# Performance work log

Measured on AMD Instinct MI355X. Metric: run time of the kernel, lower is better.

## Reference

```python
import jax, jax.numpy as jnp
import numpy as np
import math

DIM_PER_HEAD = 64

def setup_inputs() -> dict:
    key = jax.random.key(0)
    k1, k2, k3, k4 = jax.random.split(key, 4)
    B, H, S, D = 2, 16, 2048, 64
    mat1 = jax.random.normal(k1, (B, H, S, D), dtype=jnp.float32)
    mat2 = jax.random.normal(k2, (B, H, S, D), dtype=jnp.float32)
    mat3 = jax.random.normal(k3, (B, H, S, D), dtype=jnp.float32)
    bias = jax.random.normal(k4, (1, 1, S, S), dtype=jnp.float32)
    return {"mat1": mat1, "mat2": mat2, "mat3": mat3, "bias": bias}

def reference(mat1, mat2, mat3, bias) -> jnp.ndarray:
    # scale Q, scores = QK^T + bias, softmax over last dim, then @ V
    scale = 1.0 / math.sqrt(DIM_PER_HEAD)
    qk = jnp.einsum('bhqd,bhkd->bhqk', mat1 * scale, mat2)  # [B,H,S,S]
    scores = jax.nn.softmax(qk + bias, axis=-1)
    return jnp.einsum('bhqk,bhkd->bhqd', scores, mat3)
```

## Files before the change

### kernel.cpp

```cpp
#include <hip/hip_runtime.h>
#include <hip/hip_bf16.h>


#define SEQ 2048
#define DH  64
#define BHN 32
#define PST 72
#define LOG2E 1.44269504088896f

typedef __attribute__((ext_vector_type(8))) short bf16x8;
typedef __attribute__((ext_vector_type(4))) float f32x4;
typedef __attribute__((ext_vector_type(8))) short short8v;

__device__ inline short f2b(float x) {
    union { float f; unsigned u; } v; v.f = x;
    unsigned r = v.u + 0x7fff + ((v.u >> 16) & 1);
    return (short)(r >> 16);
}

__device__ inline void gl_lds16(const void* g, void* l) {
    __builtin_amdgcn_global_load_lds(
        (const __attribute__((address_space(1))) void*)g,
        (__attribute__((address_space(3))) void*)l, 16, 0, 0);
}

__global__ __launch_bounds__(256)
void prep_k(const float* __restrict__ K, short* __restrict__ Kb) {
    size_t i = ((size_t)blockIdx.x * 256 + threadIdx.x) * 8;
    f32x4 a = *(const f32x4*)(K + i);
    f32x4 b = *(const f32x4*)(K + i + 4);
    short8v t;
    #pragma unroll
    for (int j = 0; j < 4; ++j) { t[j] = f2b(a[j]); t[4 + j] = f2b(b[j]); }
    *(short8v*)(Kb + i) = t;
}

__global__ __launch_bounds__(256)
void prep_v(const float* __restrict__ V, short* __restrict__ Vt) {
    __shared__ short t[64 * 72];
    const int tid = threadIdx.x;
    const int bh = blockIdx.x >> 5, st = blockIdx.x & 31, s0 = st * 64;
    const float* Vb = V + (size_t)bh * SEQ * DH + (size_t)s0 * DH;
    #pragma unroll
    for (int i = 0; i < 4; ++i) {
        int c = tid + i * 256, s = c >> 4, c4 = c & 15;
        f32x4 v = *(const f32x4*)(Vb + s * DH + c4 * 4);
        #pragma unroll
        for (int j = 0; j < 4; ++j) t[s * 72 + c4 * 4 + j] = f2b(v[j]);
    }
    __syncthreads();
    const int d = tid >> 2, part = tid & 3;
    short8v lo, hi;
    #pragma unroll
    for (int j = 0; j < 8; ++j) {
        lo[j] = t[(part * 16 + j) * 72 + d];
        hi[j] = t[(part * 16 + 8 + j) * 72 + d];
    }
    short* outp = Vt + (size_t)bh * DH * SEQ + (size_t)d * SEQ + s0 + part * 16;
    *(short8v*)outp = lo;
    *(short8v*)(outp + 8) = hi;
}

__global__ __launch_bounds__(256, 4)
void mha_main(const float* __restrict__ Q, const float* __restrict__ Bias,
              const short* __restrict__ Kb, const short* __restrict__ Vt,
              float* __restrict__ Out)
{
    __shared__ short lds_k[64 * DH];
    __shared__ short lds_v[DH * 64];
    __shared__ short lds_p[4 * 16 * PST];

    const int tid = threadIdx.x, lane = tid & 63, wave = tid >> 6;
    const int l15 = lane & 15, l4 = lane >> 4;
    const int qb = blockIdx.x & 31, bh = blockIdx.x >> 5;
    const int q0 = qb * 64;

    const float* Qb = Q + (size_t)bh * SEQ * DH;
    const short* Kh = Kb + (size_t)bh * SEQ * DH;
    const short* Vh = Vt + (size_t)bh * DH * SEQ;
    float* Ob = Out + (size_t)bh * SEQ * DH;

    bf16x8 qf[2];
    {
        const float* qp = Qb + (size_t)(q0 + wave * 16 + l15) * DH;
        #pragma unroll
        for (int ks = 0; ks < 2; ++ks) {
            short tmp[8];
            #pragma unroll
            for (int j = 0; j < 8; ++j) tmp[j] = f2b(qp[ks * 32 + l4 * 8 + j] * 0.125f);
            qf[ks] = *reinterpret_cast<bf16x8*>(tmp);
        }
    }

    f32x4 o_acc[4];
    #pragma unroll
    for (int dt = 0; dt < 4; ++dt) o_acc[dt] = f32x4{0.f, 0.f, 0.f, 0.f};
    float l_part[4] = {0.f, 0.f, 0.f, 0.f};

    const short* kg[2]; const short* vg[2]; short* kl[2]; short* vl[2];
    #pragma unroll
    for (int p = 0; p < 2; ++p) {
        int slot = p * 256 + wave * 64 + lane;
        int r_ = slot >> 3, c_ = slot & 7;
        kg[p] = Kh + (size_t)r_ * DH + c_ * 8;
        vg[p] = Vh + (size_t)r_ * SEQ + c_ * 8;
        kl[p] = &lds_k[(size_t)(p * 256 + wave * 64) * 8];
        vl[p] = &lds_v[(size_t)(p * 256 + wave * 64) * 8];
    }
    const float* bp0 = Bias + (size_t)(q0 + wave * 16 + l4 * 4) * SEQ + l15;
    short* pw = &lds_p[wave * 16 * PST];

    for (int kt = 0; kt < SEQ / 64; ++kt) {
        const int k0 = kt * 64;
        __syncthreads();
        gl_lds16(kg[0] + (size_t)k0 * DH, kl[0]);
        gl_lds16(kg[1] + (size_t)k0 * DH, kl[1]);
        gl_lds16(vg[0] + k0, vl[0]);
        gl_lds16(vg[1] + k0, vl[1]);

        f32x4 sacc[4];
        const float* bp = bp0 + k0;
        #pragma unroll
        for (int nt = 0; nt < 4; ++nt)
            #pragma unroll
            for (int r = 0; r < 4; ++r)
                sacc[nt][r] = bp[(size_t)r * SEQ + nt * 16];

        __syncthreads();

        #pragma unroll
        for (int ks = 0; ks < 2; ++ks)
            #pragma unroll
            for (int nt = 0; nt < 4; ++nt) {
                bf16x8 kf = *(const bf16x8*)&lds_k[(nt * 16 + l15) * DH + ks * 32 + l4 * 8];
                sacc[nt] = __builtin_amdgcn_mfma_f32_16x16x32_bf16(qf[ks], kf, sacc[nt], 0, 0, 0);
            }

        #pragma unroll
        for (int r = 0; r < 4; ++r)
            #pragma unroll
            for (int nt = 0; nt < 4; ++nt) {
                float pv = __builtin_amdgcn_exp2f(sacc[nt][r] * LOG2E);
                l_part[r] += pv;
                pw[(l4 * 4 + r) * PST + nt * 16 + l15] = f2b(pv);
            }

        #pragma unroll
        for (int ks = 0; ks < 2; ++ks) {
            bf16x8 pf = *(const bf16x8*)&pw[l15 * PST + ks * 32 + l4 * 8];
            #pragma unroll
            for (int dt = 0; dt < 4; ++dt) {
                bf16x8 vf = *(const bf16x8*)&lds_v[(dt * 16 + l15) * DH + ks * 32 + l4 * 8];
                o_acc[dt] = __builtin_amdgcn_mfma_f32_16x16x32_bf16(pf, vf, o_acc[dt], 0, 0, 0);
            }
        }
    }

    #pragma unroll
    for (int r = 0; r < 4; ++r) {
        float s = l_part[r];
        #pragma unroll
        for (int m = 1; m < 16; m <<= 1) s += __shfl_xor(s, m, 64);
        l_part[r] = s;
    }

    #pragma unroll
    for (int r = 0; r < 4; ++r) {
        float inv = 1.0f / l_part[r];
        float* op = Ob + (size_t)(q0 + wave * 16 + l4 * 4 + r) * DH + l15;
        #pragma unroll
        for (int dt = 0; dt < 4; ++dt) op[dt * 16] = o_acc[dt][r] * inv;
    }
}

extern "C" void kernel_launch(void* const* d_in, const int* in_sizes, int n_in,
                              void* d_out, int out_size, void* d_ws, size_t ws_size,
                              hipStream_t stream) {
    const float* Q    = (const float*)d_in[0];
    const float* K    = (const float*)d_in[1];
    const float* V    = (const float*)d_in[2];
    const float* Bias = (const float*)d_in[3];
    float* O          = (float*)d_out;

    short* Kb = (short*)d_ws;
    short* Vt = Kb + (size_t)BHN * SEQ * DH;

    prep_k<<<dim3((BHN * SEQ * DH) / (256 * 8)), dim3(256), 0, stream>>>(K, Kb);
    prep_v<<<dim3(BHN * 32), dim3(256), 0, stream>>>(V, Vt);
    mha_main<<<dim3(BHN * 32), dim3(256), 0, stream>>>(Q, Bias, Kb, Vt, O);
}
```

Before: 196.7 us.

## XOR-swizzle LDS tiles for K, V and P; merge K/V prep kernels

```diff
diff --git a/kernel.cpp b/kernel.cpp
--- a/kernel.cpp
+++ b/kernel.cpp
@@ -5,7 +5,6 @@
 #define SEQ 2048
 #define DH  64
 #define BHN 32
-#define PST 72
 #define LOG2E 1.44269504088896f
 
 typedef __attribute__((ext_vector_type(8))) short bf16x8;
@@ -25,21 +24,27 @@
 }
 
 __global__ __launch_bounds__(256)
-void prep_k(const float* __restrict__ K, short* __restrict__ Kb) {
-    size_t i = ((size_t)blockIdx.x * 256 + threadIdx.x) * 8;
-    f32x4 a = *(const f32x4*)(K + i);
-    f32x4 b = *(const f32x4*)(K + i + 4);
-    short8v t;
-    #pragma unroll
-    for (int j = 0; j < 4; ++j) { t[j] = f2b(a[j]); t[4 + j] = f2b(b[j]); }
-    *(short8v*)(Kb + i) = t;
-}
-
-__global__ __launch_bounds__(256)
-void prep_v(const float* __restrict__ V, short* __restrict__ Vt) {
+void prep_kv(const float* __restrict__ K, const float* __restrict__ V,
+             short* __restrict__ Kb, short* __restrict__ Vt) {
     __shared__ short t[64 * 72];
     const int tid = threadIdx.x;
     const int bh = blockIdx.x >> 5, st = blockIdx.x & 31, s0 = st * 64;
+
+    {
+        const float* Kp = K + ((size_t)bh * SEQ + s0) * DH;
+        short* Ko = Kb + ((size_t)bh * SEQ + s0) * DH;
+        #pragma unroll
+        for (int i = 0; i < 2; ++i) {
+            size_t o = (size_t)(tid + i * 256) * 8;
+            f32x4 a = *(const f32x4*)(Kp + o);
+            f32x4 b = *(const f32x4*)(Kp + o + 4);
+            short8v s;
+            #pragma unroll
+            for (int j = 0; j < 4; ++j) { s[j] = f2b(a[j]); s[4 + j] = f2b(b[j]); }
+            *(short8v*)(Ko + o) = s;
+        }
+    }
+
     const float* Vb = V + (size_t)bh * SEQ * DH + (size_t)s0 * DH;
     #pragma unroll
     for (int i = 0; i < 4; ++i) {
@@ -68,7 +73,7 @@
 {
     __shared__ short lds_k[64 * DH];
     __shared__ short lds_v[DH * 64];
-    __shared__ short lds_p[4 * 16 * PST];
+    __shared__ short lds_p[4 * 16 * 64];
 
     const int tid = threadIdx.x, lane = tid & 63, wave = tid >> 6;
     const int l15 = lane & 15, l4 = lane >> 4;
@@ -101,14 +106,17 @@
     #pragma unroll
     for (int p = 0; p < 2; ++p) {
         int slot = p * 256 + wave * 64 + lane;
-        int r_ = slot >> 3, c_ = slot & 7;
-        kg[p] = Kh + (size_t)r_ * DH + c_ * 8;
-        vg[p] = Vh + (size_t)r_ * SEQ + c_ * 8;
+        int r_ = slot >> 3;
+        int c_ = slot & 7;
+        int cg = c_ ^ (r_ & 7);
+        kg[p] = Kh + (size_t)r_ * DH + cg * 8;
+        vg[p] = Vh + (size_t)r_ * SEQ + cg * 8;
         kl[p] = &lds_k[(size_t)(p * 256 + wave * 64) * 8];
         vl[p] = &lds_v[(size_t)(p * 256 + wave * 64) * 8];
     }
     const float* bp0 = Bias + (size_t)(q0 + wave * 16 + l4 * 4) * SEQ + l15;
-    short* pw = &lds_p[wave * 16 * PST];
+    short* pw = &lds_p[wave * 16 * 64];
+    const int swz = l15 & 7;
 
     for (int kt = 0; kt < SEQ / 64; ++kt) {
         const int k0 = kt * 64;
@@ -132,25 +140,31 @@
         for (int ks = 0; ks < 2; ++ks)
             #pragma unroll
             for (int nt = 0; nt < 4; ++nt) {
-                bf16x8 kf = *(const bf16x8*)&lds_k[(nt * 16 + l15) * DH + ks * 32 + l4 * 8];
+                int cc = (ks * 4 + l4) ^ swz;
+                bf16x8 kf = *(const bf16x8*)&lds_k[(nt * 16 + l15) * DH + cc * 8];
                 sacc[nt] = __builtin_amdgcn_mfma_f32_16x16x32_bf16(qf[ks], kf, sacc[nt], 0, 0, 0);
             }
 
         #pragma unroll
-        for (int r = 0; r < 4; ++r)
+        for (int r = 0; r < 4; ++r) {
+            const int prow = l4 * 4 + r;
+            const int rsw = prow & 7;
             #pragma unroll
             for (int nt = 0; nt < 4; ++nt) {
                 float pv = __builtin_amdgcn_exp2f(sacc[nt][r] * LOG2E);
                 l_part[r] += pv;
-                pw[(l4 * 4 + r) * PST + nt * 16 + l15] = f2b(pv);
+                int pc = (nt * 2 + (l15 >> 3)) ^ rsw;
+                pw[prow * 64 + pc * 8 + (l15 & 7)] = f2b(pv);
             }
+        }
 
         #pragma unroll
         for (int ks = 0; ks < 2; ++ks) {
-            bf16x8 pf = *(const bf16x8*)&pw[l15 * PST + ks * 32 + l4 * 8];
+            int cc = (ks * 4 + l4) ^ swz;
+            bf16x8 pf = *(const bf16x8*)&pw[l15 * 64 + cc * 8];
             #pragma unroll
             for (int dt = 0; dt < 4; ++dt) {
-                bf16x8 vf = *(const bf16x8*)&lds_v[(dt * 16 + l15) * DH + ks * 32 + l4 * 8];
+                bf16x8 vf = *(const bf16x8*)&lds_v[(dt * 16 + l15) * DH + cc * 8];
                 o_acc[dt] = __builtin_amdgcn_mfma_f32_16x16x32_bf16(pf, vf, o_acc[dt], 0, 0, 0);
             }
         }
@@ -185,7 +199,6 @@
     short* Kb = (short*)d_ws;
     short* Vt = Kb + (size_t)BHN * SEQ * DH;
 
-    prep_k<<<dim3((BHN * SEQ * DH) / (256 * 8)), dim3(256), 0, stream>>>(K, Kb);
-    prep_v<<<dim3(BHN * 32), dim3(256), 0, stream>>>(V, Vt);
+    prep_kv<<<dim3(BHN * 32), dim3(256), 0, stream>>>(K, V, Kb, Vt);
     mha_main<<<dim3(BHN * 32), dim3(256), 0, stream>>>(Q, Bias, Kb, Vt, O);
 }
```

Result: faster. 167.3 us (-14.9%).
